# Performance work log

Hardware: AMD Instinct MI355X
Metric: run time of the kernel (lower is better)

The kernel has to match this reference:

```python
import jax, jax.numpy as jnp
import numpy as np
from jax import lax

T, B, D_IN, H = 512, 64, 512, 1024
BETA = 1.0


def _uniform(key, shape, stdv):
    return jax.random.uniform(key, shape, jnp.float32, -stdv, stdv)


def setup_inputs() -> dict:
    key = jax.random.key(0)
    keys = jax.random.split(key, 17)
    X = jax.random.normal(keys[0], (T, B, D_IN), jnp.float32)
    stdv = 1.0 / np.sqrt(H)
    inp = {"X": X}
    # layer 0: input dim D_IN -> H ; layer 1: H -> H
    dims = [(D_IN, H), (H, H)]
    k = 1
    for li, (din, dout) in enumerate(dims):
        inp[f"ifW{li}"] = _uniform(keys[k + 0], (dout, din), stdv)
        inp[f"ifB{li}"] = _uniform(keys[k + 1], (dout,), stdv)
        inp[f"hfW{li}"] = _uniform(keys[k + 2], (dout, dout), stdv)
        inp[f"hfB{li}"] = _uniform(keys[k + 3], (dout,), stdv)
        inp[f"igW{li}"] = _uniform(keys[k + 4], (dout, din), stdv)
        inp[f"igB{li}"] = _uniform(keys[k + 5], (dout,), stdv)
        inp[f"hgW{li}"] = _uniform(keys[k + 6], (dout, dout), stdv)
        inp[f"hgB{li}"] = _uniform(keys[k + 7], (dout,), stdv)
        k += 8
    return inp


def _janet_layer(Xi, ifW, ifB, hfW, hfB, igW, igB, hgW, hgB):
    """Xi: [T, B, din] -> Y: [T, B, dout], hT: [B, dout]."""
    # Precompute input projections for all timesteps in one big GEMM each.
    Pf = jnp.einsum('tbi,hi->tbh', Xi, ifW) + ifB - BETA  # [T,B,H]
    Pg = jnp.einsum('tbi,hi->tbh', Xi, igW) + igB

    def step(h, inputs):
        pf, pg = inputs
        F = jax.nn.sigmoid(pf + h @ hfW.T + hfB)
        G = jnp.tanh(pg + h @ hgW.T + hgB)
        x = F * h + (1.0 - F) * G
        return x, x

    h0 = jnp.zeros((Xi.shape[1], ifW.shape[0]), Xi.dtype)
    hT, Y = lax.scan(step, h0, (Pf, Pg))
    return Y, hT


def reference(X, ifW0, ifB0, hfW0, hfB0, igW0, igB0, hgW0, hgB0,
              ifW1, ifB1, hfW1, hfB1, igW1, igB1, hgW1, hgB1):
    Y0, h0T = _janet_layer(X, ifW0, ifB0, hfW0, hfB0, igW0, igB0, hgW0, hgB0)
    Y1, h1T = _janet_layer(Y0, ifW1, ifB1, hfW1, hfB1, igW1, igB1, hgW1, hgB1)
    # stack_output=True, seq_dim=0: Y1 is [T, B, H]; hidden = last layer states
    return Y1
```

## Files before the change

### kernel.cpp

```cpp
#include <hip/hip_runtime.h>
#include <cstdint>

typedef short short8 __attribute__((ext_vector_type(8)));
typedef float floatx4 __attribute__((ext_vector_type(4)));

#define TS 512
#define BB 64
#define HD 1024
#define MROWS (TS * BB)

__device__ __forceinline__ unsigned short f2bf(float f) {
    uint32_t u = __float_as_uint(f);
    u += 0x7fffu + ((u >> 16) & 1u);
    return (unsigned short)(u >> 16);
}

__device__ __forceinline__ void wait_vm0() {
    asm volatile("s_waitcnt vmcnt(0)" ::: "memory");
}

__device__ __forceinline__ void raw_barrier() {
    asm volatile("s_barrier" ::: "memory");
}

__device__ __forceinline__ void ld_sc1_b128(short8& d, const unsigned short* p) {
    asm volatile("global_load_dwordx4 %0, %1, off sc0 sc1"
                 : "=&v"(d) : "v"(p));
}

#define VMWAIT(N)                                              \
    do {                                                       \
        asm volatile("s_waitcnt vmcnt(" #N ")" ::: "memory");  \
        __builtin_amdgcn_sched_barrier(0);                     \
    } while (0)

__global__ __launch_bounds__(256) void cast_f32_bf16(const float* __restrict__ s,
                                                     unsigned short* __restrict__ d, int n4) {
    int i = blockIdx.x * 256 + threadIdx.x;
    if (i >= n4) return;
    float4 v = ((const float4*)s)[i];
    ushort4 o = make_ushort4(f2bf(v.x), f2bf(v.y), f2bf(v.z), f2bf(v.w));
    ((ushort4*)d)[i] = o;
}

__global__ __launch_bounds__(256) void gemm_bt_bias(
    const unsigned short* __restrict__ A, const unsigned short* __restrict__ Bt,
    const float* __restrict__ biasF, const float* __restrict__ biasG,
    float* __restrict__ C, int M, int K)
{
    const int N = 2048;
    __shared__ unsigned short As[128 * 32];
    __shared__ unsigned short Bs[128 * 32];
    int bm = blockIdx.x * 128, bn = blockIdx.y * 128;
    int th = threadIdx.x;
    int wave = th >> 6, lane = th & 63;
    int lrow = lane & 15, quad = lane >> 4;
    int wm = (wave & 1) * 64, wn = (wave >> 1) * 64;
    const unsigned short* Ag = A + (size_t)bm * K;
    const unsigned short* Bg = Bt + (size_t)bn * K;

    floatx4 acc[4][4];
#pragma unroll
    for (int i = 0; i < 4; ++i)
#pragma unroll
        for (int j = 0; j < 4; ++j) acc[i][j] = (floatx4){0.f, 0.f, 0.f, 0.f};

    for (int k0 = 0; k0 < K; k0 += 32) {
        __syncthreads();
#pragma unroll
        for (int jj = 0; jj < 2; ++jj) {
            int c = jj * 256 + th;
            int row = c >> 2, kk = c & 3;
            int ph = (row * 4 + (kk ^ ((row >> 1) & 3))) * 8;
            uint4 va = *(const uint4*)(Ag + (size_t)row * K + k0 + kk * 8);
            uint4 vb = *(const uint4*)(Bg + (size_t)row * K + k0 + kk * 8);
            *(uint4*)(As + ph) = va;
            *(uint4*)(Bs + ph) = vb;
        }
        __syncthreads();
        short8 af[4], bfv[4];
#pragma unroll
        for (int i = 0; i < 4; ++i) {
            int r = wm + i * 16 + lrow;
            af[i] = *(const short8*)(As + (r * 4 + (quad ^ ((r >> 1) & 3))) * 8);
        }
#pragma unroll
        for (int j = 0; j < 4; ++j) {
            int r = wn + j * 16 + lrow;
            bfv[j] = *(const short8*)(Bs + (r * 4 + (quad ^ ((r >> 1) & 3))) * 8);
        }
#pragma unroll
        for (int i = 0; i < 4; ++i)
#pragma unroll
            for (int j = 0; j < 4; ++j)
                acc[i][j] = __builtin_amdgcn_mfma_f32_16x16x32_bf16(af[i], bfv[j], acc[i][j], 0, 0, 0);
    }
#pragma unroll
    for (int j = 0; j < 4; ++j) {
        int col = bn + wn + j * 16 + lrow;
        float bias = (col < 1024) ? (biasF[col] - 1.0f) : biasG[col - 1024];
#pragma unroll
        for (int i = 0; i < 4; ++i) {
            int row0 = bm + wm + i * 16 + quad * 4;
#pragma unroll
            for (int r = 0; r < 4; ++r)
                C[(size_t)(row0 + r) * N + col] = acc[i][j][r] + bias;
        }
    }
}

__global__ __launch_bounds__(256) void janet_fused(
    const float* __restrict__ P,
    const unsigned short* __restrict__ Rf0, const unsigned short* __restrict__ Rg0,
    const float* __restrict__ hbf0, const float* __restrict__ hbg0,
    const unsigned short* __restrict__ Rf1, const unsigned short* __restrict__ Rg1,
    const unsigned short* __restrict__ Wi1,
    const float* __restrict__ ifB1, const float* __restrict__ hfB1,
    const float* __restrict__ igB1, const float* __restrict__ hgB1,
    unsigned short* __restrict__ ring0,
    unsigned short* __restrict__ ring1,
    int* flags0, int* flags1,
    float* __restrict__ Yf32)
{
    __shared__ unsigned short Wl[4][16 * 1024];
    const int wg = blockIdx.x, th = threadIdx.x;
    const bool L1 = wg >= 64;
    const int w = L1 ? (wg - 64) : wg;
    const int wave = th >> 6, lane = th & 63;
    const int lrow = lane & 15, quad = lane >> 4;
    const int c0 = w * 16;
    const int col = c0 + lrow;
    const int myrow = wave * 16 + lrow;
    const int sw = lrow & 7;

    const int nchunks = L1 ? 8192 : 4096;
    for (int c = th; c < nchunks; c += 256) {
        int g = c >> 11, n = (c >> 7) & 15, k8 = c & 127;
        const unsigned short* src;
        if (L1) src = (g == 0) ? Rf1 : (g == 1) ? Rg1 : (g == 2) ? Wi1 : (Wi1 + (size_t)1024 * 1024);
        else    src = g ? Rg0 : Rf0;
        src += (size_t)(c0 + n) * 1024 + k8 * 8;
        *(uint4*)(&Wl[g][(n * 128 + (k8 ^ (n & 7))) * 8]) = *(const uint4*)src;
    }
    __syncthreads();

    float bF, bG;
    if (L1) { bF = ifB1[col] - 1.0f + hfB1[col]; bG = igB1[col] + hgB1[col]; }
    else    { bF = hbf0[col]; bG = hbg0[col]; }

    const unsigned short* w0 = &Wl[0][lrow << 10];
    const unsigned short* w1 = &Wl[1][lrow << 10];
    const unsigned short* w2 = &Wl[2][lrow << 10];
    const unsigned short* w3 = &Wl[3][lrow << 10];

    float hr[4] = {0.f, 0.f, 0.f, 0.f};

    auto pollWG = [&](int th0_, int th1_) {
        if (wave == 0) {
            int spins = 0;
            while (true) {
                int f0 = __hip_atomic_load(&flags0[lane], __ATOMIC_RELAXED,
                                           __HIP_MEMORY_SCOPE_AGENT);
                int f1 = __hip_atomic_load(&flags1[lane], __ATOMIC_RELAXED,
                                           __HIP_MEMORY_SCOPE_AGENT);
                if (__all(f0 >= th0_ && f1 >= th1_)) break;
                if (++spins > (1 << 20)) break;
                if (spins > 8) __builtin_amdgcn_s_sleep(1);
            }
        }
        raw_barrier();
    };

    auto release = [&](int* flags, int v) {
        wait_vm0();
        raw_barrier();
        if (th == 0)
            __hip_atomic_store(&flags[w], v, __ATOMIC_RELAXED, __HIP_MEMORY_SCOPE_AGENT);
    };

    if (!L1) {
        float pf[4], pg[4];
        auto pload = [&](int t, float* pfD, float* pgD) {
            size_t pbase = ((size_t)t * 64 + wave * 16 + quad * 4) * 2048 + col;
#pragma unroll
            for (int r = 0; r < 4; ++r) {
                pfD[r] = P[pbase + (size_t)r * 2048];
                pgD[r] = P[pbase + (size_t)r * 2048 + 1024];
            }
        };
        pload(0, pf, pg);

        for (int t = 0; t < TS; ++t) {
            if (t) pollWG(t, t - 7);

            const unsigned short* hs =
                ring0 + ((size_t)(t & 7) << 16) + ((size_t)myrow << 10) + (quad << 3);

            wait_vm0();
            short8 hA[8], hB[8];
            auto issue = [&](int c, short8* buf) {
#pragma unroll
                for (int i = 0; i < 8; ++i)
                    ld_sc1_b128(buf[i], hs + (((c << 3) + i) << 5));
            };
            floatx4 aF = {0.f, 0.f, 0.f, 0.f}, aG = {0.f, 0.f, 0.f, 0.f};
            auto mchunk = [&](int c, const short8* buf) {
#pragma unroll
                for (int i = 0; i < 8; ++i) {
                    int ks = (c << 3) + i;
                    int koff = ((((ks << 2) + quad) ^ sw) << 3);
                    short8 bf_ = *(const short8*)(w0 + koff);
                    short8 bg_ = *(const short8*)(w1 + koff);
                    aF = __builtin_amdgcn_mfma_f32_16x16x32_bf16(buf[i], bf_, aF, 0, 0, 0);
                    aG = __builtin_amdgcn_mfma_f32_16x16x32_bf16(buf[i], bg_, aG, 0, 0, 0);
                }
            };
            issue(0, hA);
            issue(1, hB);
            VMWAIT(8); mchunk(0, hA); issue(2, hA);
            VMWAIT(8); mchunk(1, hB); issue(3, hB);
            VMWAIT(8); mchunk(2, hA);
            VMWAIT(0); mchunk(3, hB);

            unsigned short* hd = ring0 + ((size_t)((t + 1) & 7) << 16);
#pragma unroll
            for (int r = 0; r < 4; ++r) {
                int b = wave * 16 + quad * 4 + r;
                float f = 1.f / (1.f + __expf(-(pf[r] + aF[r] + bF)));
                float xg = pg[r] + aG[r] + bG;
                xg = fminf(fmaxf(xg, -15.f), 15.f);
                float e2 = __expf(2.f * xg);
                float g = (e2 - 1.f) / (e2 + 1.f);
                float hn = f * hr[r] + (1.f - f) * g;
                hr[r] = hn;
                unsigned short hb = f2bf(hn);
                int partner = __shfl_xor((int)hb, 1, 64);
                if (!(lrow & 1)) {
                    unsigned int pk = (unsigned int)hb | ((unsigned int)partner << 16);
                    __hip_atomic_store((unsigned int*)(hd + (size_t)b * 1024 + col), pk,
                                       __ATOMIC_RELAXED, __HIP_MEMORY_SCOPE_AGENT);
                }
            }
            release(flags0, t + 1);
            if (t + 1 < TS) pload(t + 1, pf, pg);
        }
    } else {
        for (int t = 0; t < TS; ++t) {
            pollWG(t + 1, t);

            const unsigned short* ys =
                ring0 + ((size_t)((t + 1) & 7) << 16) + ((size_t)myrow << 10) + (quad << 3);
            const unsigned short* hs =
                ring1 + ((size_t)(t & 1) << 16) + ((size_t)myrow << 10) + (quad << 3);

            wait_vm0();
            short8 yA[4], yB[4], hA[4], hB[4];
            auto lcI = [&](int c, short8* yb, short8* hb) {
#pragma unroll
                for (int i = 0; i < 4; ++i) {
                    ld_sc1_b128(yb[i], ys + (((c << 2) + i) << 5));
                    ld_sc1_b128(hb[i], hs + (((c << 2) + i) << 5));
                }
            };
            floatx4 aPf = {0.f, 0.f, 0.f, 0.f}, aPg = {0.f, 0.f, 0.f, 0.f};
            floatx4 aF = {0.f, 0.f, 0.f, 0.f},  aG = {0.f, 0.f, 0.f, 0.f};
            auto mc = [&](int c, const short8* yb, const short8* hb) {
#pragma unroll
                for (int i = 0; i < 4; ++i) {
                    int ks = (c << 2) + i;
                    int koff = ((((ks << 2) + quad) ^ sw) << 3);
                    short8 wf_ = *(const short8*)(w0 + koff);
                    short8 wg_ = *(const short8*)(w1 + koff);
                    short8 wif = *(const short8*)(w2 + koff);
                    short8 wig = *(const short8*)(w3 + koff);
                    aF  = __builtin_amdgcn_mfma_f32_16x16x32_bf16(hb[i], wf_, aF, 0, 0, 0);
                    aG  = __builtin_amdgcn_mfma_f32_16x16x32_bf16(hb[i], wg_, aG, 0, 0, 0);
                    aPf = __builtin_amdgcn_mfma_f32_16x16x32_bf16(yb[i], wif, aPf, 0, 0, 0);
                    aPg = __builtin_amdgcn_mfma_f32_16x16x32_bf16(yb[i], wig, aPg, 0, 0, 0);
                }
            };
            lcI(0, yA, hA);
            lcI(1, yB, hB);
            VMWAIT(8); mc(0, yA, hA); lcI(2, yA, hA);
            VMWAIT(8); mc(1, yB, hB); lcI(3, yB, hB);
            VMWAIT(8); mc(2, yA, hA); lcI(4, yA, hA);
            VMWAIT(8); mc(3, yB, hB); lcI(5, yB, hB);
            VMWAIT(8); mc(4, yA, hA); lcI(6, yA, hA);
            VMWAIT(8); mc(5, yB, hB); lcI(7, yB, hB);
            VMWAIT(8); mc(6, yA, hA);
            VMWAIT(0); mc(7, yB, hB);

            unsigned short* hd = ring1 + ((size_t)((t + 1) & 1) << 16);
            float hn4[4];
#pragma unroll
            for (int r = 0; r < 4; ++r) {
                int b = wave * 16 + quad * 4 + r;
                float f = 1.f / (1.f + __expf(-(aPf[r] + aF[r] + bF)));
                float xg = aPg[r] + aG[r] + bG;
                xg = fminf(fmaxf(xg, -15.f), 15.f);
                float e2 = __expf(2.f * xg);
                float g = (e2 - 1.f) / (e2 + 1.f);
                float hn = f * hr[r] + (1.f - f) * g;
                hr[r] = hn;
                hn4[r] = hn;
                unsigned short hb = f2bf(hn);
                int partner = __shfl_xor((int)hb, 1, 64);
                if (!(lrow & 1)) {
                    unsigned int pk = (unsigned int)hb | ((unsigned int)partner << 16);
                    __hip_atomic_store((unsigned int*)(hd + (size_t)b * 1024 + col), pk,
                                       __ATOMIC_RELAXED, __HIP_MEMORY_SCOPE_AGENT);
                }
            }
            release(flags1, t + 1);
#pragma unroll
            for (int r = 0; r < 4; ++r) {
                int b = wave * 16 + quad * 4 + r;
                Yf32[((size_t)t * 64 + b) * 1024 + col] = hn4[r];
            }
        }
    }
}

extern "C" void kernel_launch(void* const* d_in, const int* in_sizes, int n_in,
                              void* d_out, int out_size, void* d_ws, size_t ws_size,
                              hipStream_t stream) {
    (void)in_sizes; (void)n_in; (void)out_size; (void)ws_size;
    const float* X    = (const float*)d_in[0];
    const float* ifW0 = (const float*)d_in[1];
    const float* ifB0 = (const float*)d_in[2];
    const float* hfW0 = (const float*)d_in[3];
    const float* hfB0 = (const float*)d_in[4];
    const float* igW0 = (const float*)d_in[5];
    const float* igB0 = (const float*)d_in[6];
    const float* hgW0 = (const float*)d_in[7];
    const float* hgB0 = (const float*)d_in[8];
    const float* ifW1 = (const float*)d_in[9];
    const float* ifB1 = (const float*)d_in[10];
    const float* hfW1 = (const float*)d_in[11];
    const float* hfB1 = (const float*)d_in[12];
    const float* igW1 = (const float*)d_in[13];
    const float* igB1 = (const float*)d_in[14];
    const float* hgW1 = (const float*)d_in[15];
    const float* hgB1 = (const float*)d_in[16];

    char* p = (char*)d_ws;
    auto alloc = [&](size_t bytes) {
        char* r = p; p += (bytes + 255) & ~(size_t)255; return r;
    };
    float* P            = (float*)alloc((size_t)MROWS * 2048 * 4);
    unsigned short* Xb  = (unsigned short*)alloc((size_t)MROWS * 512 * 2);
    unsigned short* W0c = (unsigned short*)alloc((size_t)2048 * 512 * 2);
    unsigned short* W1c = (unsigned short*)alloc((size_t)2048 * 1024 * 2);
    unsigned short* Rf0 = (unsigned short*)alloc((size_t)1024 * 1024 * 2);
    unsigned short* Rg0 = (unsigned short*)alloc((size_t)1024 * 1024 * 2);
    unsigned short* Rf1 = (unsigned short*)alloc((size_t)1024 * 1024 * 2);
    unsigned short* Rg1 = (unsigned short*)alloc((size_t)1024 * 1024 * 2);
    unsigned short* ring0 = (unsigned short*)alloc((size_t)8 * 64 * 1024 * 2);
    unsigned short* ring1 = (unsigned short*)alloc((size_t)2 * 64 * 1024 * 2);
    int* flags0 = (int*)alloc(4096);
    int* flags1 = (int*)alloc(4096);

    hipMemsetAsync(ring0, 0, (size_t)1048576 + 262144 + 4096 + 4096, stream);

    auto cast = [&](const float* s, unsigned short* d, size_t n) {
        int n4 = (int)(n / 4);
        cast_f32_bf16<<<dim3((n4 + 255) / 256), dim3(256), 0, stream>>>(s, d, n4);
    };
    cast(X, Xb, (size_t)MROWS * 512);
    cast(ifW0, W0c, (size_t)1024 * 512);
    cast(igW0, W0c + (size_t)1024 * 512, (size_t)1024 * 512);
    cast(ifW1, W1c, (size_t)1024 * 1024);
    cast(igW1, W1c + (size_t)1024 * 1024, (size_t)1024 * 1024);
    cast(hfW0, Rf0, (size_t)1024 * 1024);
    cast(hgW0, Rg0, (size_t)1024 * 1024);
    cast(hfW1, Rf1, (size_t)1024 * 1024);
    cast(hgW1, Rg1, (size_t)1024 * 1024);

    gemm_bt_bias<<<dim3(MROWS / 128, 16), dim3(256), 0, stream>>>(Xb, W0c, ifB0, igB0, P, MROWS, 512);

    janet_fused<<<dim3(128), dim3(256), 0, stream>>>(
        P, Rf0, Rg0, hfB0, hgB0,
        Rf1, Rg1, W1c, ifB1, hfB1, igB1, hgB1,
        ring0, ring1, flags0, flags1, (float*)d_out);
}
```

Before: 6.306 ms.

## Replace flag barriers with tagged ring entries and per-wave flags

Each hidden-state element now goes into the ring as a 32-bit word holding the bf16 value plus a timestep tag in the upper bits. Consumers check the tags on their loaded data and reload any chunk that is stale, instead of polling per-workgroup flags before every step. Per-wave flags with a looser lag check are kept only to guard against overwriting ring slots, and the workgroup barriers and waitcnt releases are removed. The ring doubles in size and layer 1 gets an 8-deep ring, which adds memory traffic and extra unpacking work in exchange for lower synchronization latency.

```diff
diff --git a/kernel.cpp b/kernel.cpp
--- a/kernel.cpp
+++ b/kernel.cpp
@@ -15,17 +15,15 @@
     return (unsigned short)(u >> 16);
 }
 
-__device__ __forceinline__ void wait_vm0() {
-    asm volatile("s_waitcnt vmcnt(0)" ::: "memory");
-}
-
-__device__ __forceinline__ void raw_barrier() {
-    asm volatile("s_barrier" ::: "memory");
-}
-
-__device__ __forceinline__ void ld_sc1_b128(short8& d, const unsigned short* p) {
-    asm volatile("global_load_dwordx4 %0, %1, off sc0 sc1"
-                 : "=&v"(d) : "v"(p));
+__device__ __forceinline__ unsigned long long ald64(const void* p) {
+    return __hip_atomic_load((const unsigned long long*)p, __ATOMIC_RELAXED,
+                             __HIP_MEMORY_SCOPE_AGENT);
+}
+
+__device__ __forceinline__ uint4 ld_sc1_u4(const unsigned int* p) {
+    uint4 d;
+    asm volatile("global_load_dwordx4 %0, %1, off sc0 sc1" : "=&v"(d) : "v"(p));
+    return d;
 }
 
 #define VMWAIT(N)                                              \
@@ -117,8 +115,8 @@
     const unsigned short* __restrict__ Wi1,
     const float* __restrict__ ifB1, const float* __restrict__ hfB1,
     const float* __restrict__ igB1, const float* __restrict__ hgB1,
-    unsigned short* __restrict__ ring0,
-    unsigned short* __restrict__ ring1,
+    unsigned int* __restrict__ ring0,
+    unsigned int* __restrict__ ring1,
     int* flags0, int* flags1,
     float* __restrict__ Yf32)
 {
@@ -155,27 +153,9 @@
 
     float hr[4] = {0.f, 0.f, 0.f, 0.f};
 
-    auto pollWG = [&](int th0_, int th1_) {
-        if (wave == 0) {
-            int spins = 0;
-            while (true) {
-                int f0 = __hip_atomic_load(&flags0[lane], __ATOMIC_RELAXED,
-                                           __HIP_MEMORY_SCOPE_AGENT);
-                int f1 = __hip_atomic_load(&flags1[lane], __ATOMIC_RELAXED,
-                                           __HIP_MEMORY_SCOPE_AGENT);
-                if (__all(f0 >= th0_ && f1 >= th1_)) break;
-                if (++spins > (1 << 20)) break;
-                if (spins > 8) __builtin_amdgcn_s_sleep(1);
-            }
-        }
-        raw_barrier();
-    };
-
-    auto release = [&](int* flags, int v) {
-        wait_vm0();
-        raw_barrier();
-        if (th == 0)
-            __hip_atomic_store(&flags[w], v, __ATOMIC_RELAXED, __HIP_MEMORY_SCOPE_AGENT);
+    auto min4 = [](unsigned long long a, unsigned long long b) {
+        int x0 = (int)a, x1 = (int)(a >> 32), x2 = (int)b, x3 = (int)(b >> 32);
+        return min(min(x0, x1), min(x2, x3));
     };
 
     if (!L1) {
@@ -191,41 +171,86 @@
         pload(0, pf, pg);
 
         for (int t = 0; t < TS; ++t) {
-            if (t) pollWG(t, t - 7);
-
-            const unsigned short* hs =
+            unsigned long long g0a = ald64(&flags0[lane * 4]);
+            unsigned long long g0b = ald64(&flags0[lane * 4 + 2]);
+            unsigned long long g1a = ald64(&flags1[lane * 4]);
+            unsigned long long g1b = ald64(&flags1[lane * 4 + 2]);
+
+            const unsigned int* hsrc =
                 ring0 + ((size_t)(t & 7) << 16) + ((size_t)myrow << 10) + (quad << 3);
-
-            wait_vm0();
-            short8 hA[8], hB[8];
-            auto issue = [&](int c, short8* buf) {
-#pragma unroll
-                for (int i = 0; i < 8; ++i)
-                    ld_sc1_b128(buf[i], hs + (((c << 3) + i) << 5));
-            };
+            const unsigned teh = (unsigned)t << 16;
             floatx4 aF = {0.f, 0.f, 0.f, 0.f}, aG = {0.f, 0.f, 0.f, 0.f};
-            auto mchunk = [&](int c, const short8* buf) {
-#pragma unroll
-                for (int i = 0; i < 8; ++i) {
-                    int ks = (c << 3) + i;
+            uint4 b[4][8];
+
+            auto issue = [&](int c, uint4* buf) {
+#pragma unroll
+                for (int i = 0; i < 4; ++i) {
+                    const unsigned int* p = hsrc + (c * 4 + i) * 32;
+                    buf[2 * i]     = ld_sc1_u4(p);
+                    buf[2 * i + 1] = ld_sc1_u4(p + 4);
+                }
+            };
+            auto chk = [&](int c, uint4* buf) {
+                int sp = 0;
+                while (true) {
+                    unsigned acc = 0;
+#pragma unroll
+                    for (int i = 0; i < 8; ++i)
+                        acc |= (buf[i].x ^ teh) | (buf[i].y ^ teh) |
+                               (buf[i].z ^ teh) | (buf[i].w ^ teh);
+                    if (__all((acc & 0xffff0000u) == 0u)) break;
+                    if (++sp > (1 << 20)) break;
+                    issue(c, buf);
+                    VMWAIT(0);
+                }
+            };
+            auto mst = [&](int c, uint4* buf) {
+#pragma unroll
+                for (int i = 0; i < 4; ++i) {
+                    int ks = c * 4 + i;
+                    uint4 q;
+                    q.x = (buf[2 * i].x & 0xffffu)     | (buf[2 * i].y << 16);
+                    q.y = (buf[2 * i].z & 0xffffu)     | (buf[2 * i].w << 16);
+                    q.z = (buf[2 * i + 1].x & 0xffffu) | (buf[2 * i + 1].y << 16);
+                    q.w = (buf[2 * i + 1].z & 0xffffu) | (buf[2 * i + 1].w << 16);
+                    short8 a = *(short8*)&q;
                     int koff = ((((ks << 2) + quad) ^ sw) << 3);
-                    short8 bf_ = *(const short8*)(w0 + koff);
-                    short8 bg_ = *(const short8*)(w1 + koff);
-                    aF = __builtin_amdgcn_mfma_f32_16x16x32_bf16(buf[i], bf_, aF, 0, 0, 0);
-                    aG = __builtin_amdgcn_mfma_f32_16x16x32_bf16(buf[i], bg_, aG, 0, 0, 0);
-                }
-            };
-            issue(0, hA);
-            issue(1, hB);
-            VMWAIT(8); mchunk(0, hA); issue(2, hA);
-            VMWAIT(8); mchunk(1, hB); issue(3, hB);
-            VMWAIT(8); mchunk(2, hA);
-            VMWAIT(0); mchunk(3, hB);
-
-            unsigned short* hd = ring0 + ((size_t)((t + 1) & 7) << 16);
+                    aF = __builtin_amdgcn_mfma_f32_16x16x32_bf16(a, *(const short8*)(w0 + koff), aF, 0, 0, 0);
+                    aG = __builtin_amdgcn_mfma_f32_16x16x32_bf16(a, *(const short8*)(w1 + koff), aG, 0, 0, 0);
+                }
+            };
+
+            issue(0, b[0]); issue(1, b[1]); issue(2, b[2]); issue(3, b[3]);
+#pragma unroll
+            for (int c = 0; c < 8; ++c) {
+                if (c <= 4) VMWAIT(24);
+                else if (c == 5) VMWAIT(16);
+                else if (c == 6) VMWAIT(8);
+                else VMWAIT(0);
+                chk(c, b[c & 3]);
+                mst(c, b[c & 3]);
+                if (c + 4 < 8) issue(c + 4, b[c & 3]);
+            }
+
+            {
+                int m0 = min4(g0a, g0b), m1 = min4(g1a, g1b);
+                int sp = 0;
+                while (!__all(m0 >= t - 6 && m1 >= t - 7)) {
+                    if (++sp > (1 << 20)) break;
+                    if (sp > 4) __builtin_amdgcn_s_sleep(1);
+                    g0a = ald64(&flags0[lane * 4]);
+                    g0b = ald64(&flags0[lane * 4 + 2]);
+                    g1a = ald64(&flags1[lane * 4]);
+                    g1b = ald64(&flags1[lane * 4 + 2]);
+                    m0 = min4(g0a, g0b); m1 = min4(g1a, g1b);
+                }
+            }
+
+            unsigned int* hd = ring0 + ((size_t)((t + 1) & 7) << 16);
+            const unsigned tagw = (unsigned)(t + 1) << 16;
 #pragma unroll
             for (int r = 0; r < 4; ++r) {
-                int b = wave * 16 + quad * 4 + r;
+                int bb = wave * 16 + quad * 4 + r;
                 float f = 1.f / (1.f + __expf(-(pf[r] + aF[r] + bF)));
                 float xg = pg[r] + aG[r] + bG;
                 xg = fminf(fmaxf(xg, -15.f), 15.f);
@@ -233,68 +258,109 @@
                 float g = (e2 - 1.f) / (e2 + 1.f);
                 float hn = f * hr[r] + (1.f - f) * g;
                 hr[r] = hn;
-                unsigned short hb = f2bf(hn);
-                int partner = __shfl_xor((int)hb, 1, 64);
-                if (!(lrow & 1)) {
-                    unsigned int pk = (unsigned int)hb | ((unsigned int)partner << 16);
-                    __hip_atomic_store((unsigned int*)(hd + (size_t)b * 1024 + col), pk,
-                                       __ATOMIC_RELAXED, __HIP_MEMORY_SCOPE_AGENT);
-                }
-            }
-            release(flags0, t + 1);
+                __hip_atomic_store(&hd[(size_t)bb * 1024 + col], tagw | (unsigned)f2bf(hn),
+                                   __ATOMIC_RELAXED, __HIP_MEMORY_SCOPE_AGENT);
+            }
+            if (lane == 0)
+                __hip_atomic_store(&flags0[w * 4 + wave], t + 1, __ATOMIC_RELAXED,
+                                   __HIP_MEMORY_SCOPE_AGENT);
             if (t + 1 < TS) pload(t + 1, pf, pg);
         }
     } else {
         for (int t = 0; t < TS; ++t) {
-            pollWG(t + 1, t);
-
-            const unsigned short* ys =
+            unsigned long long g1a = ald64(&flags1[lane * 4]);
+            unsigned long long g1b = ald64(&flags1[lane * 4 + 2]);
+
+            const unsigned int* ysrc =
                 ring0 + ((size_t)((t + 1) & 7) << 16) + ((size_t)myrow << 10) + (quad << 3);
-            const unsigned short* hs =
-                ring1 + ((size_t)(t & 1) << 16) + ((size_t)myrow << 10) + (quad << 3);
-
-            wait_vm0();
-            short8 yA[4], yB[4], hA[4], hB[4];
-            auto lcI = [&](int c, short8* yb, short8* hb) {
-#pragma unroll
-                for (int i = 0; i < 4; ++i) {
-                    ld_sc1_b128(yb[i], ys + (((c << 2) + i) << 5));
-                    ld_sc1_b128(hb[i], hs + (((c << 2) + i) << 5));
-                }
-            };
+            const unsigned int* hsrc =
+                ring1 + ((size_t)(t & 7) << 16) + ((size_t)myrow << 10) + (quad << 3);
+            const unsigned te1h = (unsigned)(t + 1) << 16;
+            const unsigned te0h = (unsigned)t << 16;
+
             floatx4 aPf = {0.f, 0.f, 0.f, 0.f}, aPg = {0.f, 0.f, 0.f, 0.f};
             floatx4 aF = {0.f, 0.f, 0.f, 0.f},  aG = {0.f, 0.f, 0.f, 0.f};
-            auto mc = [&](int c, const short8* yb, const short8* hb) {
+            uint4 yb[2][8], hb[2][8];
+
+            auto issue1 = [&](int c, uint4* yB, uint4* hB) {
 #pragma unroll
                 for (int i = 0; i < 4; ++i) {
-                    int ks = (c << 2) + i;
+                    const unsigned int* py = ysrc + (c * 4 + i) * 32;
+                    const unsigned int* ph = hsrc + (c * 4 + i) * 32;
+                    yB[2 * i]     = ld_sc1_u4(py);
+                    yB[2 * i + 1] = ld_sc1_u4(py + 4);
+                    hB[2 * i]     = ld_sc1_u4(ph);
+                    hB[2 * i + 1] = ld_sc1_u4(ph + 4);
+                }
+            };
+            auto chk1 = [&](int c, uint4* yB, uint4* hB) {
+                int sp = 0;
+                while (true) {
+                    unsigned accy = 0, acch = 0;
+#pragma unroll
+                    for (int i = 0; i < 8; ++i) {
+                        accy |= (yB[i].x ^ te1h) | (yB[i].y ^ te1h) |
+                                (yB[i].z ^ te1h) | (yB[i].w ^ te1h);
+                        acch |= (hB[i].x ^ te0h) | (hB[i].y ^ te0h) |
+                                (hB[i].z ^ te0h) | (hB[i].w ^ te0h);
+                    }
+                    if (__all(((accy | acch) & 0xffff0000u) == 0u)) break;
+                    if (++sp > (1 << 20)) break;
+                    issue1(c, yB, hB);
+                    VMWAIT(0);
+                }
+            };
+            auto mst1 = [&](int c, uint4* yB, uint4* hB) {
+#pragma unroll
+                for (int i = 0; i < 4; ++i) {
+                    int ks = c * 4 + i;
+                    uint4 qy, qh;
+                    qy.x = (yB[2 * i].x & 0xffffu)     | (yB[2 * i].y << 16);
+                    qy.y = (yB[2 * i].z & 0xffffu)     | (yB[2 * i].w << 16);
+                    qy.z = (yB[2 * i + 1].x & 0xffffu) | (yB[2 * i + 1].y << 16);
+                    qy.w = (yB[2 * i + 1].z & 0xffffu) | (yB[2 * i + 1].w << 16);
+                    qh.x = (hB[2 * i].x & 0xffffu)     | (hB[2 * i].y << 16);
+                    qh.y = (hB[2 * i].z & 0xffffu)     | (hB[2 * i].w << 16);
+                    qh.z = (hB[2 * i + 1].x & 0xffffu) | (hB[2 * i + 1].y << 16);
+                    qh.w = (hB[2 * i + 1].z & 0xffffu) | (hB[2 * i + 1].w << 16);
+                    short8 ay = *(short8*)&qy;
+                    short8 ah = *(short8*)&qh;
                     int koff = ((((ks << 2) + quad) ^ sw) << 3);
-                    short8 wf_ = *(const short8*)(w0 + koff);
-                    short8 wg_ = *(const short8*)(w1 + koff);
-                    short8 wif = *(const short8*)(w2 + koff);
-                    short8 wig = *(const short8*)(w3 + koff);
-                    aF  = __builtin_amdgcn_mfma_f32_16x16x32_bf16(hb[i], wf_, aF, 0, 0, 0);
-                    aG  = __builtin_amdgcn_mfma_f32_16x16x32_bf16(hb[i], wg_, aG, 0, 0, 0);
-                    aPf = __builtin_amdgcn_mfma_f32_16x16x32_bf16(yb[i], wif, aPf, 0, 0, 0);
-                    aPg = __builtin_amdgcn_mfma_f32_16x16x32_bf16(yb[i], wig, aPg, 0, 0, 0);
-                }
-            };
-            lcI(0, yA, hA);
-            lcI(1, yB, hB);
-            VMWAIT(8); mc(0, yA, hA); lcI(2, yA, hA);
-            VMWAIT(8); mc(1, yB, hB); lcI(3, yB, hB);
-            VMWAIT(8); mc(2, yA, hA); lcI(4, yA, hA);
-            VMWAIT(8); mc(3, yB, hB); lcI(5, yB, hB);
-            VMWAIT(8); mc(4, yA, hA); lcI(6, yA, hA);
-            VMWAIT(8); mc(5, yB, hB); lcI(7, yB, hB);
-            VMWAIT(8); mc(6, yA, hA);
-            VMWAIT(0); mc(7, yB, hB);
-
-            unsigned short* hd = ring1 + ((size_t)((t + 1) & 1) << 16);
+                    aF  = __builtin_amdgcn_mfma_f32_16x16x32_bf16(ah, *(const short8*)(w0 + koff), aF, 0, 0, 0);
+                    aG  = __builtin_amdgcn_mfma_f32_16x16x32_bf16(ah, *(const short8*)(w1 + koff), aG, 0, 0, 0);
+                    aPf = __builtin_amdgcn_mfma_f32_16x16x32_bf16(ay, *(const short8*)(w2 + koff), aPf, 0, 0, 0);
+                    aPg = __builtin_amdgcn_mfma_f32_16x16x32_bf16(ay, *(const short8*)(w3 + koff), aPg, 0, 0, 0);
+                }
+            };
+
+            issue1(0, yb[0], hb[0]); issue1(1, yb[1], hb[1]);
+#pragma unroll
+            for (int c = 0; c < 8; ++c) {
+                if (c <= 6) VMWAIT(16);
+                else VMWAIT(0);
+                chk1(c, yb[c & 1], hb[c & 1]);
+                mst1(c, yb[c & 1], hb[c & 1]);
+                if (c + 2 < 8) issue1(c + 2, yb[c & 1], hb[c & 1]);
+            }
+
+            {
+                int m1 = min4(g1a, g1b);
+                int sp = 0;
+                while (!__all(m1 >= t - 6)) {
+                    if (++sp > (1 << 20)) break;
+                    if (sp > 4) __builtin_amdgcn_s_sleep(1);
+                    g1a = ald64(&flags1[lane * 4]);
+                    g1b = ald64(&flags1[lane * 4 + 2]);
+                    m1 = min4(g1a, g1b);
+                }
+            }
+
+            unsigned int* hd = ring1 + ((size_t)((t + 1) & 7) << 16);
+            const unsigned tagw = (unsigned)(t + 1) << 16;
             float hn4[4];
 #pragma unroll
             for (int r = 0; r < 4; ++r) {
-                int b = wave * 16 + quad * 4 + r;
+                int bb = wave * 16 + quad * 4 + r;
                 float f = 1.f / (1.f + __expf(-(aPf[r] + aF[r] + bF)));
                 float xg = aPg[r] + aG[r] + bG;
                 xg = fminf(fmaxf(xg, -15.f), 15.f);
@@ -303,19 +369,16 @@
                 float hn = f * hr[r] + (1.f - f) * g;
                 hr[r] = hn;
                 hn4[r] = hn;
-                unsigned short hb = f2bf(hn);
-                int partner = __shfl_xor((int)hb, 1, 64);
-                if (!(lrow & 1)) {
-                    unsigned int pk = (unsigned int)hb | ((unsigned int)partner << 16);
-                    __hip_atomic_store((unsigned int*)(hd + (size_t)b * 1024 + col), pk,
-                                       __ATOMIC_RELAXED, __HIP_MEMORY_SCOPE_AGENT);
-                }
-            }
-            release(flags1, t + 1);
+                __hip_atomic_store(&hd[(size_t)bb * 1024 + col], tagw | (unsigned)f2bf(hn),
+                                   __ATOMIC_RELAXED, __HIP_MEMORY_SCOPE_AGENT);
+            }
+            if (lane == 0)
+                __hip_atomic_store(&flags1[w * 4 + wave], t + 1, __ATOMIC_RELAXED,
+                                   __HIP_MEMORY_SCOPE_AGENT);
 #pragma unroll
             for (int r = 0; r < 4; ++r) {
-                int b = wave * 16 + quad * 4 + r;
-                Yf32[((size_t)t * 64 + b) * 1024 + col] = hn4[r];
+                int bb = wave * 16 + quad * 4 + r;
+                Yf32[((size_t)t * 64 + bb) * 1024 + col] = hn4[r];
             }
         }
     }
@@ -355,12 +418,12 @@
     unsigned short* Rg0 = (unsigned short*)alloc((size_t)1024 * 1024 * 2);
     unsigned short* Rf1 = (unsigned short*)alloc((size_t)1024 * 1024 * 2);
     unsigned short* Rg1 = (unsigned short*)alloc((size_t)1024 * 1024 * 2);
-    unsigned short* ring0 = (unsigned short*)alloc((size_t)8 * 64 * 1024 * 2);
-    unsigned short* ring1 = (unsigned short*)alloc((size_t)2 * 64 * 1024 * 2);
+    unsigned int* ring0 = (unsigned int*)alloc((size_t)8 * 64 * 1024 * 4);
+    unsigned int* ring1 = (unsigned int*)alloc((size_t)8 * 64 * 1024 * 4);
     int* flags0 = (int*)alloc(4096);
     int* flags1 = (int*)alloc(4096);
 
-    hipMemsetAsync(ring0, 0, (size_t)1048576 + 262144 + 4096 + 4096, stream);
+    hipMemsetAsync(ring0, 0, (size_t)2 * 2097152 + 4096 + 4096, stream);
 
     auto cast = [&](const float* s, unsigned short* d, size_t n) {
         int n4 = (int)(n / 4);
```

Measured after the change: 11.35 ms. 1.8x slower.

## Replace workgroup-level flag sync with per-wave flags and polling

Applied to the files above, without the earlier changes.

Each wave now publishes and polls its own padded flag (one flag per workgroup-wave, spaced 32 ints apart) instead of wave 0 polling and then hitting a workgroup s_barrier on both acquire and release. This removes two block barriers per timestep and lets each wave proceed as soon as the matching waves of the other workgroups are done. Layer 0 now checks the layer-1 backpressure flags only every fourth step, with a smaller slack window, and the Y store moves ahead of the release. The risk is more polling traffic from four waves per block, and the ordering guarantees of the coarser sync are relaxed.

```diff
diff --git a/kernel.cpp b/kernel.cpp
--- a/kernel.cpp
+++ b/kernel.cpp
@@ -17,10 +17,6 @@
 
 __device__ __forceinline__ void wait_vm0() {
     asm volatile("s_waitcnt vmcnt(0)" ::: "memory");
-}
-
-__device__ __forceinline__ void raw_barrier() {
-    asm volatile("s_barrier" ::: "memory");
 }
 
 __device__ __forceinline__ void ld_sc1_b128(short8& d, const unsigned short* p) {
@@ -155,27 +151,30 @@
 
     float hr[4] = {0.f, 0.f, 0.f, 0.f};
 
-    auto pollWG = [&](int th0_, int th1_) {
-        if (wave == 0) {
-            int spins = 0;
-            while (true) {
-                int f0 = __hip_atomic_load(&flags0[lane], __ATOMIC_RELAXED,
+    const int fpoll = ((lane << 2) | wave) << 5;
+    const int fmine = ((w << 2) | wave) << 5;
+
+    auto pollWV = [&](int th0_, int th1_, bool useBP) {
+        int spins = 0;
+        while (true) {
+            int f0 = __hip_atomic_load(&flags0[fpoll], __ATOMIC_RELAXED,
+                                       __HIP_MEMORY_SCOPE_AGENT);
+            bool ok = f0 >= th0_;
+            if (useBP) {
+                int f1 = __hip_atomic_load(&flags1[fpoll], __ATOMIC_RELAXED,
                                            __HIP_MEMORY_SCOPE_AGENT);
-                int f1 = __hip_atomic_load(&flags1[lane], __ATOMIC_RELAXED,
-                                           __HIP_MEMORY_SCOPE_AGENT);
-                if (__all(f0 >= th0_ && f1 >= th1_)) break;
-                if (++spins > (1 << 20)) break;
-                if (spins > 8) __builtin_amdgcn_s_sleep(1);
+                ok = ok && (f1 >= th1_);
             }
-        }
-        raw_barrier();
+            if (__all(ok)) break;
+            if (++spins > (1 << 20)) break;
+            if (spins > 4) __builtin_amdgcn_s_sleep(1);
+        }
     };
 
     auto release = [&](int* flags, int v) {
         wait_vm0();
-        raw_barrier();
-        if (th == 0)
-            __hip_atomic_store(&flags[w], v, __ATOMIC_RELAXED, __HIP_MEMORY_SCOPE_AGENT);
+        if (lane == 0)
+            __hip_atomic_store(&flags[fmine], v, __ATOMIC_RELAXED, __HIP_MEMORY_SCOPE_AGENT);
     };
 
     if (!L1) {
@@ -191,7 +190,7 @@
         pload(0, pf, pg);
 
         for (int t = 0; t < TS; ++t) {
-            if (t) pollWG(t, t - 7);
+            if (t) pollWV(t, t - 4, (t & 3) == 1);
 
             const unsigned short* hs =
                 ring0 + ((size_t)(t & 7) << 16) + ((size_t)myrow << 10) + (quad << 3);
@@ -246,7 +245,7 @@
         }
     } else {
         for (int t = 0; t < TS; ++t) {
-            pollWG(t + 1, t);
+            pollWV(t + 1, t, true);
 
             const unsigned short* ys =
                 ring0 + ((size_t)((t + 1) & 7) << 16) + ((size_t)myrow << 10) + (quad << 3);
@@ -291,7 +290,6 @@
             VMWAIT(0); mc(7, yB, hB);
 
             unsigned short* hd = ring1 + ((size_t)((t + 1) & 1) << 16);
-            float hn4[4];
 #pragma unroll
             for (int r = 0; r < 4; ++r) {
                 int b = wave * 16 + quad * 4 + r;
@@ -302,7 +300,6 @@
                 float g = (e2 - 1.f) / (e2 + 1.f);
                 float hn = f * hr[r] + (1.f - f) * g;
                 hr[r] = hn;
-                hn4[r] = hn;
                 unsigned short hb = f2bf(hn);
                 int partner = __shfl_xor((int)hb, 1, 64);
                 if (!(lrow & 1)) {
@@ -310,13 +307,9 @@
                     __hip_atomic_store((unsigned int*)(hd + (size_t)b * 1024 + col), pk,
                                        __ATOMIC_RELAXED, __HIP_MEMORY_SCOPE_AGENT);
                 }
+                Yf32[((size_t)t * 64 + b) * 1024 + col] = hn;
             }
             release(flags1, t + 1);
-#pragma unroll
-            for (int r = 0; r < 4; ++r) {
-                int b = wave * 16 + quad * 4 + r;
-                Yf32[((size_t)t * 64 + b) * 1024 + col] = hn4[r];
-            }
         }
     }
 }
@@ -357,10 +350,10 @@
     unsigned short* Rg1 = (unsigned short*)alloc((size_t)1024 * 1024 * 2);
     unsigned short* ring0 = (unsigned short*)alloc((size_t)8 * 64 * 1024 * 2);
     unsigned short* ring1 = (unsigned short*)alloc((size_t)2 * 64 * 1024 * 2);
-    int* flags0 = (int*)alloc(4096);
-    int* flags1 = (int*)alloc(4096);
-
-    hipMemsetAsync(ring0, 0, (size_t)1048576 + 262144 + 4096 + 4096, stream);
+    int* flags0 = (int*)alloc(256 * 32 * 4);
+    int* flags1 = (int*)alloc(256 * 32 * 4);
+
+    hipMemsetAsync(ring0, 0, (size_t)1048576 + 262144 + 32768 + 32768, stream);
 
     auto cast = [&](const float* s, unsigned short* d, size_t n) {
         int n4 = (int)(n / 4);
```

Result: faster. 5.444 ms (-13.7%).
